# Optimization experiments

Hardware: AMD Instinct MI355X
Metric: run time of the kernel (lower is better)

## Reference

```python
import jax, jax.numpy as jnp
import numpy as np

B, S, D, H = 512, 200, 512, 8
FF = 1024          # dim_feedforward == hidden_dim
EMB, HID, FIN = 128, 1024, 64
V = 100000
QK_SCALE, ATTN_CLIP, FFN_CLIP, QKV_CLIP = 0.05, 3.0, 2.0, 1.0
PAD = 0


def _ln(x, g, b, eps=1e-6):
    m = jnp.mean(x, -1, keepdims=True)
    v = jnp.mean((x - m) ** 2, -1, keepdims=True)
    return (x - m) / jnp.sqrt(v + eps) * g + b


def setup_inputs() -> dict:
    key = jax.random.key(0)
    ks = jax.random.split(key, 32)
    n = lambda i, shape, s=0.02: (s * jax.random.normal(ks[i], shape)).astype(jnp.float32)
    emb_table = n(0, (V, D)).at[PAD].set(0.0)  # padding row zeroed
    inp = {
        'item_seq': jax.random.randint(ks[20], (B, S), 0, V),
        'user_avg_ctr': jax.random.uniform(ks[21], (B,)),
        'user_total_interactions': jax.random.uniform(ks[22], (B,)),
        'age_price': jax.random.randint(ks[23], (B,), 0, 100),
        'gender_cate': jax.random.randint(ks[24], (B,), 0, 10),
        'cms_group_id': jax.random.randint(ks[25], (B,), 0, 13),
        'emb_table': emb_table,
        'in_proj_w': n(1, (3 * D, D)),
        'out_proj_w': n(2, (D, D)),
        'out_proj_b': jnp.zeros((D,), jnp.float32),
        'ln1_g': jnp.ones((D,), jnp.float32), 'ln1_b': jnp.zeros((D,), jnp.float32),
        'ln2_g': jnp.ones((D,), jnp.float32), 'ln2_b': jnp.zeros((D,), jnp.float32),
        'lin1_w': n(3, (FF, D)), 'lin1_b': jnp.zeros((FF,), jnp.float32),
        'lin2_w': n(4, (D, FF)), 'lin2_b': jnp.zeros((D,), jnp.float32),
        'age_tab': n(5, (100, EMB)), 'gender_tab': n(6, (10, EMB)), 'cms_tab': n(7, (13, EMB)),
        'ctr_w': n(8, (EMB, 1)), 'ctr_b': jnp.zeros((EMB,), jnp.float32),
        'ti_w': n(9, (EMB, 1)), 'ti_b': jnp.zeros((EMB,), jnp.float32),
        'mlp1_w': n(10, (HID, D + 5 * EMB)), 'mlp1_b': jnp.zeros((HID,), jnp.float32),
        'mlp2_w': n(11, (FIN, HID)), 'mlp2_b': jnp.zeros((FIN,), jnp.float32),
    }
    return inp


def reference(item_seq, user_avg_ctr, user_total_interactions, age_price, gender_cate,
              cms_group_id, emb_table, in_proj_w, out_proj_w, out_proj_b,
              ln1_g, ln1_b, ln2_g, ln2_b, lin1_w, lin1_b, lin2_w, lin2_b,
              age_tab, gender_tab, cms_tab, ctr_w, ctr_b, ti_w, ti_b,
              mlp1_w, mlp1_b, mlp2_w, mlp2_b):
    dk = D // H
    pad = item_seq == PAD  # [B,S] key padding mask
    x = jnp.clip(emb_table[item_seq] * 0.5, -1.0, 1.0)  # [B,S,D]

    # ---- custom self-attention block (no in_proj bias, heavy clamping) ----
    qw, kw, vw = in_proj_w[:D], in_proj_w[D:2 * D], in_proj_w[2 * D:]
    q = jnp.clip(x @ qw.T, -QKV_CLIP, QKV_CLIP)
    k = jnp.clip(x @ kw.T, -QKV_CLIP, QKV_CLIP)
    v = jnp.clip(x @ vw.T, -QKV_CLIP, QKV_CLIP)
    q = q.reshape(B, S, H, dk).transpose(0, 2, 1, 3)
    k = k.reshape(B, S, H, dk).transpose(0, 2, 1, 3)
    v = v.reshape(B, S, H, dk).transpose(0, 2, 1, 3)
    scores = jnp.einsum('bhqd,bhkd->bhqk', q, k) / (np.float32(np.sqrt(dk)) * QK_SCALE)
    scores = jnp.clip(scores, -ATTN_CLIP, ATTN_CLIP)
    scores = jnp.where(pad[:, None, None, :], -1e9, scores)
    w = jax.nn.softmax(scores, axis=-1)  # dropout is identity in eval
    x2 = jnp.einsum('bhqk,bhkd->bhqd', w, v).transpose(0, 2, 1, 3).reshape(B, S, D)
    x2 = jnp.clip(x2 @ out_proj_w.T + out_proj_b, -ATTN_CLIP, ATTN_CLIP)
    sa = _ln(x + x2, ln1_g, ln1_b)          # norm1 inside overridden _sa_block
    x = _ln(x + sa, ln1_g, ln1_b)           # base post-norm wraps norm1 again

    # ---- FFN block with clamps ----
    h = jax.nn.relu(jnp.clip(x @ lin1_w.T + lin1_b, -FFN_CLIP, FFN_CLIP))
    f2 = jnp.clip(h @ lin2_w.T + lin2_b, -FFN_CLIP, FFN_CLIP)
    ff = _ln(x + f2, ln2_g, ln2_b)          # norm2 inside overridden _ff_block
    x = _ln(x + ff, ln2_g, ln2_b)           # base wraps norm2 again

    seq_out = jnp.clip(x, -5.0, 5.0)
    m = (~pad).astype(seq_out.dtype)[:, :, None]
    seq_rep = jnp.clip((seq_out * m).sum(1) / (m.sum(1) + 1e-8), -5.0, 5.0)  # [B,D]

    ape = age_tab[age_price]
    ge = gender_tab[gender_cate]
    ce = cms_tab[cms_group_id]
    ctr = user_avg_ctr[:, None] @ ctr_w.T + ctr_b
    ti = user_total_interactions[:, None] @ ti_w.T + ti_b
    u = jnp.concatenate([seq_rep, ctr, ti, ape, ge, ce], axis=-1)  # [B, D+5*EMB]
    return jax.nn.relu(u @ mlp1_w.T + mlp1_b) @ mlp2_w.T + mlp2_b  # [B, FIN]
```

## Files before the change

kernel.cpp:

```cpp
#include <hip/hip_runtime.h>
#include <hip/hip_bf16.h>
#include <stdint.h>

typedef __attribute__((ext_vector_type(8))) short short8;
typedef __attribute__((ext_vector_type(4))) float f32x4;
typedef unsigned short u16;

#define MFMA16(a,b,c) __builtin_amdgcn_mfma_f32_16x16x32_bf16((a),(b),(c),0,0,0)

__device__ __forceinline__ u16 f2bf(float f) {
  unsigned int u = __float_as_uint(f);
  return (u16)((u + 0x7FFFu + ((u >> 16) & 1u)) >> 16);
}
__device__ __forceinline__ float bf2f(u16 h) {
  return __uint_as_float(((unsigned int)h) << 16);
}
__device__ __forceinline__ float clampf(float v, float lo, float hi) {
  return fminf(fmaxf(v, lo), hi);
}
__device__ __forceinline__ void gl2lds16(const u16* g, u16* l) {
  __builtin_amdgcn_global_load_lds(
      (const __attribute__((address_space(1))) unsigned int*)g,
      (__attribute__((address_space(3))) unsigned int*)(uintptr_t)l,
      16, 0, 0);
}

__global__ __launch_bounds__(256) void cvt_bf16_kernel(
    const float* __restrict__ src, u16* __restrict__ dst, int n) {
  for (int i = blockIdx.x*256 + threadIdx.x; i < n; i += gridDim.x*256)
    dst[i] = f2bf(src[i]);
}

__global__ __launch_bounds__(256) void embed_kernel(
    const int* __restrict__ iseq, const float* __restrict__ emb,
    u16* __restrict__ xb) {
  int gid = blockIdx.x*256 + threadIdx.x;
  int m = gid >> 7;
  int c = (gid & 127) * 4;
  int item = iseq[m];
  float4 e = *(const float4*)&emb[(size_t)item*512 + c];
  ushort4 hb;
  hb.x = f2bf(clampf(e.x*0.5f, -1.f, 1.f));
  hb.y = f2bf(clampf(e.y*0.5f, -1.f, 1.f));
  hb.z = f2bf(clampf(e.z*0.5f, -1.f, 1.f));
  hb.w = f2bf(clampf(e.w*0.5f, -1.f, 1.f));
  *(ushort4*)&xb[(size_t)m*512 + c] = hb;
}

__global__ __launch_bounds__(256) void cnt_kernel(
    const int* __restrict__ item_seq, float* __restrict__ cnt) {
  __shared__ int sred[4];
  int b = blockIdx.x, tid = threadIdx.x;
  int lane = tid & 63, wv = tid >> 6;
  int c = 0;
  if (tid < 200) c = (item_seq[b*200 + tid] != 0) ? 1 : 0;
  #pragma unroll
  for (int m = 1; m <= 32; m <<= 1) c += __shfl_xor(c, m);
  if (lane == 0) sred[wv] = c;
  __syncthreads();
  if (tid == 0) cnt[b] = (float)(sred[0]+sred[1]+sred[2]+sred[3]);
}

template <int MODE>
__global__ __launch_bounds__(256)
void gemm_bt(const u16* __restrict__ A, const u16* __restrict__ Bw,
             const float* __restrict__ bias, int K, int Nt, int swz,
             u16* __restrict__ outB, u16* __restrict__ QKV, long long projStride) {
  __shared__ __align__(16) u16 As[128*32];
  __shared__ __align__(16) u16 Bs[128*32];
  const int tid = threadIdx.x;
  const int lane = tid & 63;
  const int wv = tid >> 6;
  const int id = blockIdx.x;
  int mt, nt2;
  if (swz) { mt = (id / (8*Nt))*8 + (id & 7); nt2 = (id >> 3) % Nt; }
  else     { mt = id / Nt;                    nt2 = id % Nt; }
  const int m0 = mt * 128;
  const int n0 = nt2 * 128;
  const int wm = wv >> 1, wn = wv & 1;

  const f32x4 fz = {0.f, 0.f, 0.f, 0.f};
  f32x4 acc[4][4];
  #pragma unroll
  for (int i = 0; i < 4; ++i)
    #pragma unroll
    for (int j = 0; j < 4; ++j) acc[i][j] = fz;

  const int arow = wv*32 + (lane >> 2);
  const int acol = (lane & 3) * 8;
  const u16* Ag = A  + (size_t)(m0 + arow)*K + acol;
  const u16* Bg = Bw + (size_t)(n0 + arow)*K + acol;
  u16* AsW = &As[(wv*32)*32];
  u16* BsW = &Bs[(wv*32)*32];

  const int fr = lane & 15;
  const int fk = (lane >> 4) * 8;
  const int KT = K >> 5;

  for (int kt = 0; kt < KT; ++kt) {
    const int k0 = kt * 32;
    gl2lds16(Ag + k0, AsW);
    gl2lds16(Ag + (size_t)16*K + k0, AsW + 16*32);
    gl2lds16(Bg + k0, BsW);
    gl2lds16(Bg + (size_t)16*K + k0, BsW + 16*32);
    __syncthreads();
    short8 af[4], bv[4];
    #pragma unroll
    for (int t = 0; t < 4; ++t) {
      af[t] = *(const short8*)&As[(wm*64 + t*16 + fr)*32 + fk];
      bv[t] = *(const short8*)&Bs[(wn*64 + t*16 + fr)*32 + fk];
    }
    #pragma unroll
    for (int mt2 = 0; mt2 < 4; ++mt2)
      #pragma unroll
      for (int nt = 0; nt < 4; ++nt)
        acc[mt2][nt] = MFMA16(af[mt2], bv[nt], acc[mt2][nt]);
    __syncthreads();
  }

  if (MODE == 0) {
    #pragma unroll
    for (int nt = 0; nt < 4; ++nt) {
      const int col = n0 + wn*64 + nt*16 + (lane & 15);
      const unsigned proj = (unsigned)col >> 9;
      const unsigned hh   = ((unsigned)col >> 6) & 7u;
      const unsigned dk   = (unsigned)col & 63u;
      u16* base = QKV + (size_t)proj*projStride + (size_t)hh*12800 + dk;
      #pragma unroll
      for (int mt2 = 0; mt2 < 4; ++mt2) {
        const int rowb = m0 + wm*64 + mt2*16 + ((lane >> 4) << 2);
        int b = rowb / 200;
        int s = rowb - b*200;
        size_t addr = (size_t)b*102400 + (size_t)s*64;
        #pragma unroll
        for (int r = 0; r < 4; ++r) {
          base[addr] = f2bf(clampf(acc[mt2][nt][r], -1.f, 1.f));
          ++s; addr += 64;
          if (s == 200) { s = 0; addr += 102400 - 12800; }
        }
      }
    }
  } else {
    const int N = (MODE == 2) ? 1024 : 512;
    #pragma unroll
    for (int nt = 0; nt < 4; ++nt) {
      const int col = n0 + wn*64 + nt*16 + (lane & 15);
      const float bvs = bias[col];
      #pragma unroll
      for (int mt2 = 0; mt2 < 4; ++mt2) {
        const int rowb = m0 + wm*64 + mt2*16 + ((lane >> 4) << 2);
        #pragma unroll
        for (int r = 0; r < 4; ++r) {
          const int row = rowb + r;
          float v = acc[mt2][nt][r] + bvs;
          if (MODE == 1)      v = clampf(v, -3.f, 3.f);
          else if (MODE == 2) v = fmaxf(clampf(v, -2.f, 2.f), 0.f);
          else                v = clampf(v, -2.f, 2.f);
          outB[(size_t)row*N + col] = f2bf(v);
        }
      }
    }
  }
}

__global__ __launch_bounds__(256)
void attn_kernel(const u16* __restrict__ Q, const u16* __restrict__ K,
                 const u16* __restrict__ V, const int* __restrict__ iseq,
                 u16* __restrict__ x2b) {
  __shared__ __align__(16) u16 Ks[208*72];
  __shared__ __align__(16) u16 Vs[64*232];
  __shared__ __align__(16) u16 Ps[4][16*40];
  __shared__ float msk[208];

  const int tid = threadIdx.x, lane = tid & 63, wv = tid >> 6;
  const unsigned bid = blockIdx.x;
  const int h = bid & 7;
  const int b = bid >> 3;
  const size_t bh = (size_t)b*8 + h;
  const u16* Kg = K + bh*12800;
  const u16* Vg = V + bh*12800;
  const u16* Qg = Q + bh*12800;

  for (int c = tid; c < 3200; c += 256) {
    int row = c >> 4, q = c & 15;
    *(ushort4*)&Ks[row*72 + q*4] = *(const ushort4*)&Kg[row*64 + q*4];
  }
  for (int c = tid; c < 3200; c += 256) {
    int s = c >> 4, dq = (c & 15) * 4;
    ushort4 v4 = *(const ushort4*)&Vg[s*64 + dq];
    Vs[(dq+0)*232 + s] = v4.x;
    Vs[(dq+1)*232 + s] = v4.y;
    Vs[(dq+2)*232 + s] = v4.z;
    Vs[(dq+3)*232 + s] = v4.w;
  }
  for (int c = tid; c < 2048; c += 256) {
    int dk = c >> 5, s2 = 200 + (c & 31);
    Vs[dk*232 + s2] = 0;
  }
  for (int t = tid; t < 208; t += 256)
    msk[t] = (t < 200 && iseq[b*200 + t] != 0) ? 1.f : 0.f;
  __syncthreads();

  const int colk = lane & 15;
  const int fk8 = (lane >> 4) * 8;
  const int prow = (lane >> 4) * 4;
  const f32x4 fz = {0.f,0.f,0.f,0.f};

  for (int qb = 0; qb < 4; ++qb) {
    const int qrow = qb*64 + wv*16 + (lane & 15);
    const int qsrc = qrow < 200 ? qrow : 199;
    short8 qa0 = *(const short8*)&Qg[(size_t)qsrc*64 + fk8];
    short8 qa1 = *(const short8*)&Qg[(size_t)qsrc*64 + 32 + fk8];
    f32x4 oacc[4];
    #pragma unroll
    for (int nt = 0; nt < 4; ++nt) oacc[nt] = fz;
    float rs[4] = {0.f,0.f,0.f,0.f};

    for (int kt2 = 0; kt2 < 7; ++kt2) {
      #pragma unroll
      for (int half = 0; half < 2; ++half) {
        const int stile = kt2*2 + half;
        if (stile < 13) {
          const int key = stile*16 + colk;
          short8 kb0 = *(const short8*)&Ks[key*72 + fk8];
          short8 kb1 = *(const short8*)&Ks[key*72 + 32 + fk8];
          f32x4 sc = fz;
          sc = MFMA16(qa0, kb0, sc);
          sc = MFMA16(qa1, kb1, sc);
          const float mk = msk[key];
          #pragma unroll
          for (int r = 0; r < 4; ++r) {
            float p = __expf(clampf(sc[r]*2.5f, -3.f, 3.f)) * mk;
            rs[r] += p;
            Ps[wv][(prow + r)*40 + half*16 + colk] = f2bf(p);
          }
        } else {
          #pragma unroll
          for (int r = 0; r < 4; ++r)
            Ps[wv][(prow + r)*40 + half*16 + colk] = 0;
        }
      }
      asm volatile("s_waitcnt lgkmcnt(0)" ::: "memory");
      short8 pa = *(const short8*)&Ps[wv][(lane & 15)*40 + fk8];
      const int kb32 = kt2*32;
      #pragma unroll
      for (int nt = 0; nt < 4; ++nt) {
        short8 vb = *(const short8*)&Vs[(nt*16 + colk)*232 + kb32 + fk8];
        oacc[nt] = MFMA16(pa, vb, oacc[nt]);
      }
      asm volatile("s_waitcnt lgkmcnt(0)" ::: "memory");
    }

    #pragma unroll
    for (int m = 1; m <= 8; m <<= 1)
      #pragma unroll
      for (int r = 0; r < 4; ++r) rs[r] += __shfl_xor(rs[r], m);

    const int srow = qb*64 + wv*16 + prow;
    #pragma unroll
    for (int r = 0; r < 4; ++r) {
      const int s = srow + r;
      if (s < 200) {
        const float inv = rs[r] > 0.f ? 1.f/rs[r] : 0.f;
        const size_t base = ((size_t)b*200 + s)*512 + h*64;
        #pragma unroll
        for (int nt = 0; nt < 4; ++nt)
          x2b[base + nt*16 + colk] = f2bf(oacc[nt][r] * inv);
      }
    }
  }
}

__global__ __launch_bounds__(256)
void ln1_kernel(const u16* __restrict__ xb, const u16* __restrict__ x2b,
                const float* __restrict__ g, const float* __restrict__ bb,
                u16* __restrict__ xnb) {
  const int lane = threadIdx.x & 63, wv = threadIdx.x >> 6;
  const size_t t = (size_t)blockIdx.x*4 + wv;
  const int c0 = lane*4, c1 = 256 + lane*4;
  ushort4 xa = *(const ushort4*)&xb[t*512 + c0];
  ushort4 xc = *(const ushort4*)&xb[t*512 + c1];
  ushort4 ha = *(const ushort4*)&x2b[t*512 + c0];
  ushort4 hc = *(const ushort4*)&x2b[t*512 + c1];
  float xv[8] = {bf2f(xa.x),bf2f(xa.y),bf2f(xa.z),bf2f(xa.w),
                 bf2f(xc.x),bf2f(xc.y),bf2f(xc.z),bf2f(xc.w)};
  float tv[8] = {xv[0]+bf2f(ha.x), xv[1]+bf2f(ha.y), xv[2]+bf2f(ha.z), xv[3]+bf2f(ha.w),
                 xv[4]+bf2f(hc.x), xv[5]+bf2f(hc.y), xv[6]+bf2f(hc.z), xv[7]+bf2f(hc.w)};
  float s1 = 0.f, s2 = 0.f;
  #pragma unroll
  for (int i = 0; i < 8; ++i) { s1 += tv[i]; s2 += tv[i]*tv[i]; }
  #pragma unroll
  for (int m = 1; m <= 32; m <<= 1) { s1 += __shfl_xor(s1, m); s2 += __shfl_xor(s2, m); }
  float mean = s1*(1.f/512.f);
  float inv = 1.f/sqrtf(s2*(1.f/512.f) - mean*mean + 1e-6f);
  float4 ga = *(const float4*)(g + c0), gc = *(const float4*)(g + c1);
  float4 ba = *(const float4*)(bb + c0), bc = *(const float4*)(bb + c1);
  float gv[8] = {ga.x,ga.y,ga.z,ga.w, gc.x,gc.y,gc.z,gc.w};
  float bv[8] = {ba.x,ba.y,ba.z,ba.w, bc.x,bc.y,bc.z,bc.w};
  float uv[8]; float s3 = 0.f, s4 = 0.f;
  #pragma unroll
  for (int i = 0; i < 8; ++i) {
    float sa = (tv[i]-mean)*inv*gv[i] + bv[i];
    uv[i] = xv[i] + sa;
    s3 += uv[i]; s4 += uv[i]*uv[i];
  }
  #pragma unroll
  for (int m = 1; m <= 32; m <<= 1) { s3 += __shfl_xor(s3, m); s4 += __shfl_xor(s4, m); }
  float mean2 = s3*(1.f/512.f);
  float inv2 = 1.f/sqrtf(s4*(1.f/512.f) - mean2*mean2 + 1e-6f);
  ushort4 o0, o1;
  o0.x = f2bf((uv[0]-mean2)*inv2*gv[0] + bv[0]);
  o0.y = f2bf((uv[1]-mean2)*inv2*gv[1] + bv[1]);
  o0.z = f2bf((uv[2]-mean2)*inv2*gv[2] + bv[2]);
  o0.w = f2bf((uv[3]-mean2)*inv2*gv[3] + bv[3]);
  o1.x = f2bf((uv[4]-mean2)*inv2*gv[4] + bv[4]);
  o1.y = f2bf((uv[5]-mean2)*inv2*gv[5] + bv[5]);
  o1.z = f2bf((uv[6]-mean2)*inv2*gv[6] + bv[6]);
  o1.w = f2bf((uv[7]-mean2)*inv2*gv[7] + bv[7]);
  *(ushort4*)&xnb[t*512 + c0] = o0;
  *(ushort4*)&xnb[t*512 + c1] = o1;
}

__global__ __launch_bounds__(256)
void ln2_kernel(const u16* __restrict__ xnb, const u16* __restrict__ f2b,
                const float* __restrict__ g, const float* __restrict__ bb,
                const int* __restrict__ iseq, float* __restrict__ seq_acc) {
  const int tid = threadIdx.x, lane = tid & 63, wv = tid >> 6;
  const int q = blockIdx.x, bl = blockIdx.y;
  const int c8 = lane*8;
  float gv[8], bv[8];
  *(float4*)&gv[0] = *(const float4*)(g + c8);
  *(float4*)&gv[4] = *(const float4*)(g + c8 + 4);
  *(float4*)&bv[0] = *(const float4*)(bb + c8);
  *(float4*)&bv[4] = *(const float4*)(bb + c8 + 4);
  float acc[8] = {};
  for (int i = wv; i < 50; i += 4) {
    const int s = q*50 + i;
    const size_t row = (size_t)bl*200 + s;
    short8 xh = *(const short8*)&xnb[row*512 + c8];
    short8 yh = *(const short8*)&f2b[row*512 + c8];
    float xv[8], tv[8];
    #pragma unroll
    for (int j = 0; j < 8; ++j) {
      xv[j] = bf2f((u16)xh[j]);
      tv[j] = xv[j] + bf2f((u16)yh[j]);
    }
    float s1 = 0.f, s2 = 0.f;
    #pragma unroll
    for (int j = 0; j < 8; ++j) { s1 += tv[j]; s2 += tv[j]*tv[j]; }
    #pragma unroll
    for (int m = 1; m <= 32; m <<= 1) { s1 += __shfl_xor(s1,m); s2 += __shfl_xor(s2,m); }
    float mean = s1*(1.f/512.f);
    float inv = 1.f/sqrtf(s2*(1.f/512.f) - mean*mean + 1e-6f);
    float uv[8]; float s3 = 0.f, s4 = 0.f;
    #pragma unroll
    for (int j = 0; j < 8; ++j) {
      uv[j] = xv[j] + (tv[j]-mean)*inv*gv[j] + bv[j];
      s3 += uv[j]; s4 += uv[j]*uv[j];
    }
    #pragma unroll
    for (int m = 1; m <= 32; m <<= 1) { s3 += __shfl_xor(s3,m); s4 += __shfl_xor(s4,m); }
    float mean2 = s3*(1.f/512.f);
    float inv2 = 1.f/sqrtf(s4*(1.f/512.f) - mean2*mean2 + 1e-6f);
    if (iseq[row] != 0) {
      #pragma unroll
      for (int j = 0; j < 8; ++j)
        acc[j] += clampf((uv[j]-mean2)*inv2*gv[j] + bv[j], -5.f, 5.f);
    }
  }
  float* dst = &seq_acc[(((size_t)bl*4 + q)*4 + wv)*512 + c8];
  *(float4*)&dst[0] = *(float4*)&acc[0];
  *(float4*)&dst[4] = *(float4*)&acc[4];
}

__global__ __launch_bounds__(256)
void build_u_kernel(const float* __restrict__ seq_acc, const float* __restrict__ cnt,
                    const float* __restrict__ uac, const float* __restrict__ uti,
                    const int* __restrict__ age, const int* __restrict__ gen,
                    const int* __restrict__ cms,
                    const float* __restrict__ age_tab, const float* __restrict__ gen_tab,
                    const float* __restrict__ cms_tab,
                    const float* __restrict__ ctr_w, const float* __restrict__ ctr_b,
                    const float* __restrict__ ti_w, const float* __restrict__ ti_b,
                    float* __restrict__ u) {
  const int b = blockIdx.x;
  for (int j = threadIdx.x; j < 1152; j += 256) {
    float v;
    if (j < 512) {
      float ssum = 0.f;
      #pragma unroll
      for (int p = 0; p < 16; ++p) ssum += seq_acc[((size_t)b*16 + p)*512 + j];
      v = clampf(ssum / (cnt[b] + 1e-8f), -5.f, 5.f);
    }
    else if (j < 640)  { int e = j-512;  v = uac[b]*ctr_w[e] + ctr_b[e]; }
    else if (j < 768)  { int e = j-640;  v = uti[b]*ti_w[e] + ti_b[e]; }
    else if (j < 896)  { int e = j-768;  v = age_tab[age[b]*128 + e]; }
    else if (j < 1024) { int e = j-896;  v = gen_tab[gen[b]*128 + e]; }
    else               { int e = j-1024; v = cms_tab[cms[b]*128 + e]; }
    u[(size_t)b*1152 + j] = v;
  }
}

__global__ __launch_bounds__(256)
void mlp1_kernel(const float* __restrict__ u, const float* __restrict__ w,
                 const float* __restrict__ bias, float* __restrict__ h1) {
  __shared__ __align__(16) float As[64][36];
  __shared__ __align__(16) float Wt[32][68];
  const int tid = threadIdx.x;
  const int m0 = blockIdx.x*64, n0 = blockIdx.y*64;
  const int tm = tid >> 4, tn = tid & 15;
  float acc[4][4] = {};
  for (int k0 = 0; k0 < 1152; k0 += 32) {
    for (int c = tid; c < 512; c += 256) {
      int row = c >> 3, q = c & 7;
      *(float4*)&As[row][q*4] = *(const float4*)&u[(size_t)(m0+row)*1152 + k0 + q*4];
      float4 wv4 = *(const float4*)&w[(size_t)(n0+row)*1152 + k0 + q*4];
      Wt[q*4+0][row] = wv4.x; Wt[q*4+1][row] = wv4.y;
      Wt[q*4+2][row] = wv4.z; Wt[q*4+3][row] = wv4.w;
    }
    __syncthreads();
    #pragma unroll
    for (int kk = 0; kk < 32; ++kk) {
      float av[4], bw[4];
      #pragma unroll
      for (int i = 0; i < 4; ++i) av[i] = As[tm*4+i][kk];
      #pragma unroll
      for (int j = 0; j < 4; ++j) bw[j] = Wt[kk][tn*4+j];
      #pragma unroll
      for (int i = 0; i < 4; ++i)
        #pragma unroll
        for (int j = 0; j < 4; ++j) acc[i][j] += av[i]*bw[j];
    }
    __syncthreads();
  }
  #pragma unroll
  for (int i = 0; i < 4; ++i)
    #pragma unroll
    for (int j = 0; j < 4; ++j) {
      int n = n0 + tn*4 + j;
      h1[(size_t)(m0 + tm*4 + i)*1024 + n] = fmaxf(acc[i][j] + bias[n], 0.f);
    }
}

__global__ __launch_bounds__(256)
void mlp2_kernel(const float* __restrict__ h1, const float* __restrict__ w,
                 const float* __restrict__ bias, float* __restrict__ out) {
  const int tid = threadIdx.x;
  const int m = blockIdx.x*4 + (tid >> 6);
  const int n = tid & 63;
  const float4* hr = (const float4*)(h1 + (size_t)m*1024);
  const float4* wr = (const float4*)(w + (size_t)n*1024);
  float acc = 0.f;
  for (int k4 = 0; k4 < 256; ++k4) {
    float4 a = hr[k4], bw = wr[k4];
    acc += a.x*bw.x + a.y*bw.y + a.z*bw.z + a.w*bw.w;
  }
  out[(size_t)m*64 + n] = acc + bias[n];
}

extern "C" void kernel_launch(void* const* d_in, const int* in_sizes, int n_in,
                              void* d_out, int out_size, void* d_ws, size_t ws_size,
                              hipStream_t stream) {
  (void)in_sizes; (void)n_in; (void)out_size;
  const int*   item_seq   = (const int*)d_in[0];
  const float* uac        = (const float*)d_in[1];
  const float* uti        = (const float*)d_in[2];
  const int*   age        = (const int*)d_in[3];
  const int*   gen        = (const int*)d_in[4];
  const int*   cms        = (const int*)d_in[5];
  const float* emb        = (const float*)d_in[6];
  const float* in_proj_w  = (const float*)d_in[7];
  const float* out_proj_w = (const float*)d_in[8];
  const float* out_proj_b = (const float*)d_in[9];
  const float* ln1_g = (const float*)d_in[10];
  const float* ln1_b = (const float*)d_in[11];
  const float* ln2_g = (const float*)d_in[12];
  const float* ln2_b = (const float*)d_in[13];
  const float* lin1_w = (const float*)d_in[14];
  const float* lin1_b = (const float*)d_in[15];
  const float* lin2_w = (const float*)d_in[16];
  const float* lin2_b = (const float*)d_in[17];
  const float* age_tab = (const float*)d_in[18];
  const float* gen_tab = (const float*)d_in[19];
  const float* cms_tab = (const float*)d_in[20];
  const float* ctr_w = (const float*)d_in[21];
  const float* ctr_b = (const float*)d_in[22];
  const float* ti_w  = (const float*)d_in[23];
  const float* ti_b  = (const float*)d_in[24];
  const float* mlp1_w = (const float*)d_in[25];
  const float* mlp1_b = (const float*)d_in[26];
  const float* mlp2_w = (const float*)d_in[27];
  const float* mlp2_b = (const float*)d_in[28];

  const long long TAILB = 25430016LL;
  int CB = 32;
  if      ((long long)ws_size >= 512LL*1024000 + TAILB) CB = 512;
  else if ((long long)ws_size >= 128LL*1024000 + TAILB) CB = 128;
  else if ((long long)ws_size >=  64LL*1024000 + TAILB) CB = 64;
  const long long R = (long long)CB * 204800;

  char* ws = (char*)d_ws;
  u16* xb   = (u16*)(ws);
  u16* x2b  = (u16*)(ws + R);
  u16* Qb   = (u16*)(ws + 2*R);
  u16* Kb   = (u16*)(ws + 3*R);
  u16* Vrb  = (u16*)(ws + 4*R);
  u16* x2o  = Qb;
  u16* xnb  = Kb;
  u16* f2b  = Vrb;
  u16* hbuf = (u16*)(ws);
  char* tail = ws + 5*R;
  float* seq_acc = (float*)(tail);
  float* cnt     = (float*)(tail + 16777216);
  float* u       = (float*)(tail + 16779264);
  float* h1      = (float*)(tail + 19138560);
  u16*   wqkv    = (u16*)(tail + 21235712);
  u16*   wout    = (u16*)(tail + 22808576);
  u16*   wl1     = (u16*)(tail + 23332864);
  u16*   wl2     = (u16*)(tail + 24381440);

  cvt_bf16_kernel<<<768, 256, 0, stream>>>(in_proj_w, wqkv, 1536*512);
  cvt_bf16_kernel<<<256, 256, 0, stream>>>(out_proj_w, wout, 512*512);
  cvt_bf16_kernel<<<512, 256, 0, stream>>>(lin1_w, wl1, 1024*512);
  cvt_bf16_kernel<<<512, 256, 0, stream>>>(lin2_w, wl2, 512*1024);
  cnt_kernel<<<512, 256, 0, stream>>>(item_seq, cnt);

  const int nch = 512 / CB;
  const int Mc  = CB * 200;
  const int Mt  = Mc / 128;
  const int swz = (Mt % 8 == 0) ? 1 : 0;
  const long long projStride = (long long)CB * 102400;
  for (int ch = 0; ch < nch; ++ch) {
    const int* iseq = item_seq + (size_t)ch*CB*200;
    embed_kernel<<<Mc/2, 256, 0, stream>>>(iseq, emb, xb);
    gemm_bt<0><<<Mt*12, 256, 0, stream>>>(xb, wqkv, nullptr, 512, 12, swz,
                                          nullptr, Qb, projStride);
    attn_kernel<<<CB*8, 256, 0, stream>>>(Qb, Kb, Vrb, iseq, x2b);
    gemm_bt<1><<<Mt*4, 256, 0, stream>>>(x2b, wout, out_proj_b, 512, 4, swz,
                                         x2o, nullptr, 0);
    ln1_kernel<<<Mc/4, 256, 0, stream>>>(xb, x2o, ln1_g, ln1_b, xnb);
    gemm_bt<2><<<Mt*8, 256, 0, stream>>>(xnb, wl1, lin1_b, 512, 8, swz,
                                         hbuf, nullptr, 0);
    gemm_bt<3><<<Mt*4, 256, 0, stream>>>(hbuf, wl2, lin2_b, 1024, 4, swz,
                                         f2b, nullptr, 0);
    ln2_kernel<<<dim3(4, CB), 256, 0, stream>>>(xnb, f2b, ln2_g, ln2_b, iseq,
                                                seq_acc + (size_t)ch*CB*8192);
  }

  build_u_kernel<<<512, 256, 0, stream>>>(seq_acc, cnt, uac, uti, age, gen, cms,
                                          age_tab, gen_tab, cms_tab,
                                          ctr_w, ctr_b, ti_w, ti_b, u);
  mlp1_kernel<<<dim3(8, 16), 256, 0, stream>>>(u, mlp1_w, mlp1_b, h1);
  mlp2_kernel<<<128, 256, 0, stream>>>(h1, mlp2_w, mlp2_b, (float*)d_out);
}
```

Before: 1.587 ms.

## Rewrite GEMM as 256x256-tile, 8-wave kernel with double-buffered swizzled LDS pipeline

The bf16 GEMM now uses 256x256 output tiles, 512 threads and K-steps of 64. Global-to-LDS loads are double-buffered and interleaved with four quadrant MFMA phases, using XOR-swizzled LDS addressing, explicit vmcnt waits and s_setprio. The aim is to hide load latency, cut LDS bank conflicts and raise arithmetic intensity per tile. In exchange the kernel needs far more LDS and registers (128 accumulator floats per thread), leaves fewer blocks for small M, and the hand-counted waitcnt and tile-edge logic is fragile.

Result: faster. 1.526 ms (-3.9%).

```diff
diff --git a/kernel.cpp b/kernel.cpp
--- a/kernel.cpp
+++ b/kernel.cpp
@@ -61,80 +61,163 @@
   if (tid == 0) cnt[b] = (float)(sred[0]+sred[1]+sred[2]+sred[3]);
 }
 
+#define BAR() asm volatile("s_barrier" ::: "memory")
+
+__device__ __forceinline__ void stage_half(const char* gsrc0, size_t rstride,
+                                           u16* lhalf, int wv, int lane) {
+  #pragma unroll
+  for (int j = 0; j < 2; ++j) {
+    const int o   = j*8192 + wv*1024 + lane*16;
+    const int row = o >> 7;
+    const int cb  = (o & 127) ^ ((row & 7) << 4);
+    gl2lds16((const u16*)(gsrc0 + (size_t)row*rstride + cb),
+             (u16*)((char*)lhalf + j*8192 + wv*1024));
+  }
+}
+
+__device__ __forceinline__ short8 ldsfrag(const u16* slot, int row, int kb) {
+  return *(const short8*)((const char*)slot + row*128 + (kb ^ ((row & 7) << 4)));
+}
+
+#define QUAD(AH, NB)                                                          \
+  _Pragma("unroll")                                                           \
+  for (int i = 0; i < 4; ++i)                                                 \
+    _Pragma("unroll")                                                         \
+    for (int nf = 0; nf < 2; ++nf)                                            \
+      _Pragma("unroll")                                                       \
+      for (int ks = 0; ks < 2; ++ks)                                          \
+        acc[(AH)*4 + i][(NB)*2 + nf] =                                        \
+            MFMA16(af[AH][i][ks], bf[nf][ks], acc[(AH)*4 + i][(NB)*2 + nf]);
+
 template <int MODE>
-__global__ __launch_bounds__(256)
+__global__ __launch_bounds__(512)
 void gemm_bt(const u16* __restrict__ A, const u16* __restrict__ Bw,
              const float* __restrict__ bias, int K, int Nt, int swz,
              u16* __restrict__ outB, u16* __restrict__ QKV, long long projStride) {
-  __shared__ __align__(16) u16 As[128*32];
-  __shared__ __align__(16) u16 Bs[128*32];
-  const int tid = threadIdx.x;
+  __shared__ __align__(16) u16 As[2][256*64];
+  __shared__ __align__(16) u16 Bs[2][256*64];
+  const int tid  = threadIdx.x;
   const int lane = tid & 63;
-  const int wv = tid >> 6;
-  const int id = blockIdx.x;
+  const int wv   = tid >> 6;
+  const int wm   = wv >> 2;
+  const int wn   = wv & 3;
+  const int id   = blockIdx.x;
   int mt, nt2;
   if (swz) { mt = (id / (8*Nt))*8 + (id & 7); nt2 = (id >> 3) % Nt; }
   else     { mt = id / Nt;                    nt2 = id % Nt; }
-  const int m0 = mt * 128;
-  const int n0 = nt2 * 128;
-  const int wm = wv >> 1, wn = wv & 1;
+  const int m0 = mt * 256;
+  const int n0 = nt2 * 256;
+  const int KT = K >> 6;
+
+  const char* Abase = (const char*)(A  + (size_t)m0*K);
+  const char* Bbase = (const char*)(Bw + (size_t)n0*K);
+  const size_t rs = (size_t)K * 2;
+
+  const int r16 = lane & 15;
+  const int q4  = lane >> 4;
 
   const f32x4 fz = {0.f, 0.f, 0.f, 0.f};
-  f32x4 acc[4][4];
-  #pragma unroll
-  for (int i = 0; i < 4; ++i)
+  f32x4 acc[8][4];
+  #pragma unroll
+  for (int i = 0; i < 8; ++i)
     #pragma unroll
     for (int j = 0; j < 4; ++j) acc[i][j] = fz;
 
-  const int arow = wv*32 + (lane >> 2);
-  const int acol = (lane & 3) * 8;
-  const u16* Ag = A  + (size_t)(m0 + arow)*K + acol;
-  const u16* Bg = Bw + (size_t)(n0 + arow)*K + acol;
-  u16* AsW = &As[(wv*32)*32];
-  u16* BsW = &Bs[(wv*32)*32];
-
-  const int fr = lane & 15;
-  const int fk = (lane >> 4) * 8;
-  const int KT = K >> 5;
-
-  for (int kt = 0; kt < KT; ++kt) {
-    const int k0 = kt * 32;
-    gl2lds16(Ag + k0, AsW);
-    gl2lds16(Ag + (size_t)16*K + k0, AsW + 16*32);
-    gl2lds16(Bg + k0, BsW);
-    gl2lds16(Bg + (size_t)16*K + k0, BsW + 16*32);
-    __syncthreads();
-    short8 af[4], bv[4];
-    #pragma unroll
-    for (int t = 0; t < 4; ++t) {
-      af[t] = *(const short8*)&As[(wm*64 + t*16 + fr)*32 + fk];
-      bv[t] = *(const short8*)&Bs[(wn*64 + t*16 + fr)*32 + fk];
-    }
-    #pragma unroll
-    for (int mt2 = 0; mt2 < 4; ++mt2)
-      #pragma unroll
-      for (int nt = 0; nt < 4; ++nt)
-        acc[mt2][nt] = MFMA16(af[mt2], bv[nt], acc[mt2][nt]);
-    __syncthreads();
+  stage_half(Abase,            rs, &As[0][0],      wv, lane);
+  stage_half(Abase + 128*rs,   rs, &As[0][128*64], wv, lane);
+  stage_half(Bbase,            rs, &Bs[0][0],      wv, lane);
+  stage_half(Bbase + 128*rs,   rs, &Bs[0][128*64], wv, lane);
+  if (KT > 1) {
+    stage_half(Abase + 128,          rs, &As[1][0],      wv, lane);
+    stage_half(Abase + 128*rs + 128, rs, &As[1][128*64], wv, lane);
+    asm volatile("s_waitcnt vmcnt(4)" ::: "memory");
+  } else {
+    asm volatile("s_waitcnt vmcnt(0)" ::: "memory");
+  }
+  BAR();
+
+  short8 af[2][4][2];
+  short8 bf[2][2];
+
+  for (int t = 0; t < KT; ++t) {
+    const int cur = t & 1;
+    const u16* Asl = As[cur];
+    const u16* Bsl = Bs[cur];
+    u16* Bnx = Bs[cur ^ 1];
+    u16* Anx = As[cur];
+    const char* Bg1 = Bbase + (size_t)(t+1)*128;
+    const char* Ag2 = Abase + (size_t)(t+2)*128;
+    const bool s1 = (t+1 < KT);
+    const bool s2 = (t+2 < KT);
+
+    #pragma unroll
+    for (int i = 0; i < 4; ++i)
+      #pragma unroll
+      for (int ks = 0; ks < 2; ++ks)
+        af[0][i][ks] = ldsfrag(Asl, wm*128 + i*16 + r16, ks*64 + q4*16);
+    #pragma unroll
+    for (int nf = 0; nf < 2; ++nf)
+      #pragma unroll
+      for (int ks = 0; ks < 2; ++ks)
+        bf[nf][ks] = ldsfrag(Bsl, wn*64 + nf*16 + r16, ks*64 + q4*16);
+    if (s1) stage_half(Bg1, rs, Bnx, wv, lane);
+    BAR();
+    __builtin_amdgcn_s_setprio(1);
+    QUAD(0, 0);
+    __builtin_amdgcn_s_setprio(0);
+    BAR();
+
+    #pragma unroll
+    for (int i = 0; i < 4; ++i)
+      #pragma unroll
+      for (int ks = 0; ks < 2; ++ks)
+        af[1][i][ks] = ldsfrag(Asl, wm*128 + 64 + i*16 + r16, ks*64 + q4*16);
+    if (s1) stage_half(Bg1 + 128*rs, rs, Bnx + 128*64, wv, lane);
+    BAR();
+    __builtin_amdgcn_s_setprio(1);
+    QUAD(1, 0);
+    __builtin_amdgcn_s_setprio(0);
+    BAR();
+
+    #pragma unroll
+    for (int nf = 0; nf < 2; ++nf)
+      #pragma unroll
+      for (int ks = 0; ks < 2; ++ks)
+        bf[nf][ks] = ldsfrag(Bsl, wn*64 + 32 + nf*16 + r16, ks*64 + q4*16);
+    if (s2) stage_half(Ag2, rs, Anx, wv, lane);
+    BAR();
+    __builtin_amdgcn_s_setprio(1);
+    QUAD(1, 1);
+    __builtin_amdgcn_s_setprio(0);
+    BAR();
+
+    if (s2) stage_half(Ag2 + 128*rs, rs, Anx + 128*64, wv, lane);
+    if (t < KT-2)       asm volatile("s_waitcnt vmcnt(4)" ::: "memory");
+    else if (t == KT-2) asm volatile("s_waitcnt vmcnt(0)" ::: "memory");
+    BAR();
+    __builtin_amdgcn_s_setprio(1);
+    QUAD(0, 1);
+    __builtin_amdgcn_s_setprio(0);
+    BAR();
   }
 
   if (MODE == 0) {
     #pragma unroll
-    for (int nt = 0; nt < 4; ++nt) {
-      const int col = n0 + wn*64 + nt*16 + (lane & 15);
+    for (int nf = 0; nf < 4; ++nf) {
+      const int col = n0 + wn*64 + nf*16 + r16;
       const unsigned proj = (unsigned)col >> 9;
       const unsigned hh   = ((unsigned)col >> 6) & 7u;
       const unsigned dk   = (unsigned)col & 63u;
       u16* base = QKV + (size_t)proj*projStride + (size_t)hh*12800 + dk;
       #pragma unroll
-      for (int mt2 = 0; mt2 < 4; ++mt2) {
-        const int rowb = m0 + wm*64 + mt2*16 + ((lane >> 4) << 2);
+      for (int mi = 0; mi < 8; ++mi) {
+        const int rowb = m0 + wm*128 + mi*16 + q4*4;
         int b = rowb / 200;
         int s = rowb - b*200;
         size_t addr = (size_t)b*102400 + (size_t)s*64;
         #pragma unroll
         for (int r = 0; r < 4; ++r) {
-          base[addr] = f2bf(clampf(acc[mt2][nt][r], -1.f, 1.f));
+          base[addr] = f2bf(clampf(acc[mi][nf][r], -1.f, 1.f));
           ++s; addr += 64;
           if (s == 200) { s = 0; addr += 102400 - 12800; }
         }
@@ -143,16 +226,16 @@
   } else {
     const int N = (MODE == 2) ? 1024 : 512;
     #pragma unroll
-    for (int nt = 0; nt < 4; ++nt) {
-      const int col = n0 + wn*64 + nt*16 + (lane & 15);
+    for (int nf = 0; nf < 4; ++nf) {
+      const int col = n0 + wn*64 + nf*16 + r16;
       const float bvs = bias[col];
       #pragma unroll
-      for (int mt2 = 0; mt2 < 4; ++mt2) {
-        const int rowb = m0 + wm*64 + mt2*16 + ((lane >> 4) << 2);
+      for (int mi = 0; mi < 8; ++mi) {
+        const int rowb = m0 + wm*128 + mi*16 + q4*4;
         #pragma unroll
         for (int r = 0; r < 4; ++r) {
           const int row = rowb + r;
-          float v = acc[mt2][nt][r] + bvs;
+          float v = acc[mi][nf][r] + bvs;
           if (MODE == 1)      v = clampf(v, -3.f, 3.f);
           else if (MODE == 2) v = fmaxf(clampf(v, -2.f, 2.f), 0.f);
           else                v = clampf(v, -2.f, 2.f);
@@ -527,21 +610,21 @@
 
   const int nch = 512 / CB;
   const int Mc  = CB * 200;
-  const int Mt  = Mc / 128;
+  const int Mt  = Mc / 256;
   const int swz = (Mt % 8 == 0) ? 1 : 0;
   const long long projStride = (long long)CB * 102400;
   for (int ch = 0; ch < nch; ++ch) {
     const int* iseq = item_seq + (size_t)ch*CB*200;
     embed_kernel<<<Mc/2, 256, 0, stream>>>(iseq, emb, xb);
-    gemm_bt<0><<<Mt*12, 256, 0, stream>>>(xb, wqkv, nullptr, 512, 12, swz,
-                                          nullptr, Qb, projStride);
+    gemm_bt<0><<<Mt*6, 512, 0, stream>>>(xb, wqkv, nullptr, 512, 6, swz,
+                                         nullptr, Qb, projStride);
     attn_kernel<<<CB*8, 256, 0, stream>>>(Qb, Kb, Vrb, iseq, x2b);
-    gemm_bt<1><<<Mt*4, 256, 0, stream>>>(x2b, wout, out_proj_b, 512, 4, swz,
+    gemm_bt<1><<<Mt*2, 512, 0, stream>>>(x2b, wout, out_proj_b, 512, 2, swz,
                                          x2o, nullptr, 0);
     ln1_kernel<<<Mc/4, 256, 0, stream>>>(xb, x2o, ln1_g, ln1_b, xnb);
-    gemm_bt<2><<<Mt*8, 256, 0, stream>>>(xnb, wl1, lin1_b, 512, 8, swz,
+    gemm_bt<2><<<Mt*4, 512, 0, stream>>>(xnb, wl1, lin1_b, 512, 4, swz,
                                          hbuf, nullptr, 0);
-    gemm_bt<3><<<Mt*4, 256, 0, stream>>>(hbuf, wl2, lin2_b, 1024, 4, swz,
+    gemm_bt<3><<<Mt*2, 512, 0, stream>>>(hbuf, wl2, lin2_b, 1024, 2, swz,
                                          f2b, nullptr, 0);
     ln2_kernel<<<dim3(4, CB), 256, 0, stream>>>(xnb, f2b, ln2_g, ln2_b, iseq,
                                                 seq_acc + (size_t)ch*CB*8192);
```
